# Kernel tuning notes

Hardware: AMD Instinct MI355X
Metric: run time of the kernel (lower is better)

The kernel has to match this reference:

```python
import jax, jax.numpy as jnp
import numpy as np

V, D, K = 400000, 300, 10

def setup_inputs() -> dict:
    key = jax.random.key(0)
    k1, k2 = jax.random.split(key)
    word2vec = jax.random.normal(k1, (V, D), dtype=jnp.float32)  # embedding table
    w = jax.random.normal(k2, (D,), dtype=jnp.float32)           # query vector
    return {"word2vec": word2vec, "w": w, "k": K}

def reference(word2vec, w, k):
    # cosine similarity: (word2vec @ w) / (||rows|| * ||w||), matching torch eps placement
    dots = word2vec @ w                                          # [V]
    row_norms = jnp.sqrt(jnp.sum(word2vec * word2vec, axis=1) + 1e-9)  # [V]
    q_norm = jnp.sqrt(jnp.sum(w * w))
    cos = dots / (row_norms * q_norm)                            # [V]
    vals, topk = jax.lax.top_k(cos, k)                           # top-k neighbors
    return vals, topk
```

## Files before the change

kernel.cpp:

```cpp
#include <hip/hip_runtime.h>

#define D    300
#define NF4  75
#define K    10
#define WPB  4
#define GPB  16
#define NBLOCKS 2048
#define CPT  20

__device__ __forceinline__ float d4(float4 a, float4 b) {
    return a.x*b.x + a.y*b.y + a.z*b.z + a.w*b.w;
}

__global__ __launch_bounds__(256) void cos_topk_partial(
    const float* __restrict__ emb, const float* __restrict__ wvec,
    float* __restrict__ cand_v, int* __restrict__ cand_i,
    int V, int totalGroups)
{
    const int tid  = threadIdx.x;
    const int lane = tid & 63;
    const int wid  = tid >> 6;
    const int l16  = lane & 15;
    const int rg   = lane >> 4;

    const float4* w4p = (const float4*)wvec;
    float4 w0 = w4p[l16];
    float4 w1 = w4p[l16 + 16];
    float4 w2 = w4p[l16 + 32];
    float4 w3 = w4p[l16 + 48];
    float4 w4t = make_float4(0.f, 0.f, 0.f, 0.f);
    if (l16 < NF4 - 64) w4t = w4p[l16 + 64];

    float qsq = d4(w0,w0) + d4(w1,w1) + d4(w2,w2) + d4(w3,w3) + d4(w4t,w4t);
    #pragma unroll
    for (int m = 8; m >= 1; m >>= 1) qsq += __shfl_xor(qsq, m, 64);
    const float qn = sqrtf(qsq);

    float tv[K]; int ti[K];
    #pragma unroll
    for (int j = 0; j < K; ++j) { tv[j] = -1e30f; ti[j] = 0; }

    const int g0 = (blockIdx.x * WPB + wid) * 4 + rg;
    for (int r = g0; r < V; r += totalGroups) {
        const float4* rp = (const float4*)(emb + (size_t)r * D);
        float4 a0 = rp[l16];
        float4 a1 = rp[l16 + 16];
        float4 a2 = rp[l16 + 32];
        float4 a3 = rp[l16 + 48];
        float4 a4 = make_float4(0.f, 0.f, 0.f, 0.f);
        if (l16 < NF4 - 64) a4 = rp[l16 + 64];

        float da = d4(a0, w0) + d4(a1, w1);
        float db = d4(a2, w2) + d4(a3, w3) + d4(a4, w4t);
        float sa = d4(a0, a0) + d4(a1, a1);
        float sb = d4(a2, a2) + d4(a3, a3) + d4(a4, a4);
        float dot = da + db;
        float sq  = sa + sb;

        #pragma unroll
        for (int m = 8; m >= 1; m >>= 1) {
            dot += __shfl_xor(dot, m, 64);
            sq  += __shfl_xor(sq,  m, 64);
        }
        float c = dot / (sqrtf(sq + 1e-9f) * qn);

        if (c > tv[K-1]) {
            tv[K-1] = c; ti[K-1] = r;
            #pragma unroll
            for (int j = K-1; j > 0; --j) {
                if (tv[j] > tv[j-1]) {
                    float t = tv[j]; tv[j] = tv[j-1]; tv[j-1] = t;
                    int   u = ti[j]; ti[j] = ti[j-1]; ti[j-1] = u;
                }
            }
        }
    }

    __shared__ float sv[GPB * K];
    __shared__ int   si[GPB * K];
    if (l16 == 0) {
        const int gidx = wid * 4 + rg;
        #pragma unroll
        for (int j = 0; j < K; ++j) { sv[gidx*K + j] = tv[j]; si[gidx*K + j] = ti[j]; }
    }
    __syncthreads();
    if (tid == 0) {
        float bv[K]; int bi[K];
        #pragma unroll
        for (int j = 0; j < K; ++j) { bv[j] = -1e30f; bi[j] = 0; }
        for (int t = 0; t < GPB * K; ++t) {
            float c = sv[t]; int r = si[t];
            if (c > bv[K-1]) {
                bv[K-1] = c; bi[K-1] = r;
                #pragma unroll
                for (int j = K-1; j > 0; --j) {
                    if (bv[j] > bv[j-1]) {
                        float t2 = bv[j]; bv[j] = bv[j-1]; bv[j-1] = t2;
                        int   u2 = bi[j]; bi[j] = bi[j-1]; bi[j-1] = u2;
                    }
                }
            }
        }
        #pragma unroll
        for (int j = 0; j < K; ++j) {
            cand_v[blockIdx.x*K + j] = bv[j];
            cand_i[blockIdx.x*K + j] = bi[j];
        }
    }
}

__global__ __launch_bounds__(1024) void topk_final(
    const float* __restrict__ cand_v, const int* __restrict__ cand_i,
    int nc, float* __restrict__ out)
{
    __shared__ float rv[16];
    __shared__ int   rp[16];
    __shared__ float s_bv;
    __shared__ int   s_bp;

    const int tid  = threadIdx.x;
    const int lane = tid & 63;
    const int wid  = tid >> 6;

    float v[CPT];
    #pragma unroll
    for (int t = 0; t < CPT; ++t) {
        int idx = tid + t * 1024;
        v[t] = (idx < nc) ? cand_v[idx] : -3e38f;
    }

    for (int p = 0; p < K; ++p) {
        float bestv = -3e38f; int bestpos = 0x7fffffff;
        #pragma unroll
        for (int t = 0; t < CPT; ++t) {
            if (v[t] > bestv) { bestv = v[t]; bestpos = tid + t * 1024; }
        }
        #pragma unroll
        for (int m = 32; m >= 1; m >>= 1) {
            float ov = __shfl_xor(bestv, m, 64);
            int   op = __shfl_xor(bestpos, m, 64);
            if (ov > bestv || (ov == bestv && op < bestpos)) { bestv = ov; bestpos = op; }
        }
        if (lane == 0) { rv[wid] = bestv; rp[wid] = bestpos; }
        __syncthreads();
        if (tid == 0) {
            float bv = rv[0]; int bp = rp[0];
            for (int i = 1; i < 16; ++i)
                if (rv[i] > bv || (rv[i] == bv && rp[i] < bp)) { bv = rv[i]; bp = rp[i]; }
            s_bv = bv; s_bp = bp;
            out[p]     = bv;
            out[K + p] = (float)cand_i[bp];
        }
        __syncthreads();
        const int wbp = s_bp;
        #pragma unroll
        for (int t = 0; t < CPT; ++t) {
            if (tid + t * 1024 == wbp) v[t] = -3e38f;
        }
        __syncthreads();
    }
}

extern "C" void kernel_launch(void* const* d_in, const int* in_sizes, int n_in,
                              void* d_out, int out_size, void* d_ws, size_t ws_size,
                              hipStream_t stream) {
    const float* emb  = (const float*)d_in[0];
    const float* wvec = (const float*)d_in[1];
    const int V = in_sizes[0] / D;

    int nblocks = NBLOCKS;
    size_t need = (size_t)nblocks * K * 8;
    if (need > ws_size) {
        nblocks = (int)(ws_size / (K * 8));
        if (nblocks < 1) nblocks = 1;
    }

    float* cand_v = (float*)d_ws;
    int*   cand_i = (int*)((float*)d_ws + (size_t)nblocks * K);

    cos_topk_partial<<<nblocks, 256, 0, stream>>>(emb, wvec, cand_v, cand_i,
                                                  V, nblocks * GPB);
    topk_final<<<1, 1024, 0, stream>>>(cand_v, cand_i, nblocks * K, (float*)d_out);
}
```

Before: 133.3 us.

## Split cosine scoring from top-k into three kernels with double-buffered row loads

The fused score-plus-top-k kernel is replaced by three kernels. The first writes every cosine score to workspace, prefetching the next row into registers while the current one is reduced. The second runs a block-level top-k over contiguous slices in 64 blocks, and the third merges 640 candidates. The aim is to strip the per-row insertion-sort branch out of the bandwidth-bound streaming loop and to overlap loads with compute. In exchange it adds a 1.6 MB score write and read-back plus an extra launch, and it assumes the workspace is large and V/s is at least 2.

```diff
diff --git a/kernel.cpp b/kernel.cpp
--- a/kernel.cpp
+++ b/kernel.cpp
@@ -6,22 +6,29 @@
 #define WPB  4
 #define GPB  16
 #define NBLOCKS 2048
-#define CPT  20
+#define NGROUPS (NBLOCKS * GPB)
+
+#define P2_BLOCKS  64
+#define P2_THREADS 1024
+#define P2_CPT     7
 
 __device__ __forceinline__ float d4(float4 a, float4 b) {
     return a.x*b.x + a.y*b.y + a.z*b.z + a.w*b.w;
 }
 
-__global__ __launch_bounds__(256) void cos_topk_partial(
+#define RED16(x) { x += __shfl_xor(x, 8, 64); x += __shfl_xor(x, 4, 64); \
+                   x += __shfl_xor(x, 2, 64); x += __shfl_xor(x, 1, 64); }
+
+__global__ __launch_bounds__(256) void cos_all(
     const float* __restrict__ emb, const float* __restrict__ wvec,
-    float* __restrict__ cand_v, int* __restrict__ cand_i,
-    int V, int totalGroups)
+    float* __restrict__ score, int V, int s)
 {
     const int tid  = threadIdx.x;
     const int lane = tid & 63;
     const int wid  = tid >> 6;
     const int l16  = lane & 15;
     const int rg   = lane >> 4;
+    const bool tl  = (l16 < NF4 - 64);
 
     const float4* w4p = (const float4*)wvec;
     float4 w0 = w4p[l16];
@@ -29,112 +36,151 @@
     float4 w2 = w4p[l16 + 32];
     float4 w3 = w4p[l16 + 48];
     float4 w4t = make_float4(0.f, 0.f, 0.f, 0.f);
-    if (l16 < NF4 - 64) w4t = w4p[l16 + 64];
-
-    float qsq = d4(w0,w0) + d4(w1,w1) + d4(w2,w2) + d4(w3,w3) + d4(w4t,w4t);
+    if (tl) w4t = w4p[l16 + 64];
+
+    float qsq = d4(w0,w0)+d4(w1,w1)+d4(w2,w2)+d4(w3,w3)+d4(w4t,w4t);
+    RED16(qsq);
+    const float qn = sqrtf(qsq);
+
+    const int g0 = (blockIdx.x * WPB + wid) * 4 + rg;
+    const size_t stepF4 = (size_t)s * NF4;
+
+    const float4* pA = (const float4*)emb + (size_t)g0 * NF4;
+    const float4* pB = pA + stepF4;
+
+    float4 A0,A1,A2,A3,A4, B0,B1,B2,B3,B4;
+    A4 = make_float4(0.f,0.f,0.f,0.f);
+    B4 = make_float4(0.f,0.f,0.f,0.f);
+
+#define LOADROW(P, C0,C1,C2,C3,C4) \
+    { C0 = (P)[l16]; C1 = (P)[l16+16]; C2 = (P)[l16+32]; C3 = (P)[l16+48]; \
+      if (tl) C4 = (P)[l16+64]; }
+
+#define DOTSQ(C0,C1,C2,C3,C4, DOT, SQ)                       \
+    float DOT, SQ;                                           \
+    {   float _da = d4(C0,w0) + d4(C1,w1);                   \
+        float _db = d4(C2,w2) + d4(C3,w3) + d4(C4,w4t);      \
+        float _sa = d4(C0,C0) + d4(C1,C1);                   \
+        float _sb = d4(C2,C2) + d4(C3,C3) + d4(C4,C4);       \
+        DOT = _da + _db; SQ = _sa + _sb; }
+
+#define FINISH(DOT, SQ, ROW)                                 \
+    { RED16(DOT); RED16(SQ);                                 \
+      float _c = DOT / (sqrtf(SQ + 1e-9f) * qn);             \
+      if (l16 == 0) score[ROW] = _c; }
+
+    LOADROW(pA, A0,A1,A2,A3,A4);
+    LOADROW(pB, B0,B1,B2,B3,B4);
+
+    int rowA = g0;
+    int rowB = g0 + s;
+    const int nfull = V / s;
+
+    for (int it = 0; it < nfull/2 - 1; ++it) {
+        {
+            DOTSQ(A0,A1,A2,A3,A4, dA, sA);
+            pA += 2*stepF4;
+            LOADROW(pA, A0,A1,A2,A3,A4);
+            FINISH(dA, sA, rowA);
+            rowA += 2*s;
+        }
+        {
+            DOTSQ(B0,B1,B2,B3,B4, dB, sB);
+            pB += 2*stepF4;
+            LOADROW(pB, B0,B1,B2,B3,B4);
+            FINISH(dB, sB, rowB);
+            rowB += 2*s;
+        }
+    }
+
+    {
+        DOTSQ(A0,A1,A2,A3,A4, dA, sA);
+        const bool hasTail = (rowA + 2*s) < V;
+        if (hasTail) { pA += 2*stepF4; LOADROW(pA, A0,A1,A2,A3,A4); }
+        FINISH(dA, sA, rowA);
+        {
+            DOTSQ(B0,B1,B2,B3,B4, dB, sB);
+            FINISH(dB, sB, rowB);
+        }
+        if (hasTail) {
+            DOTSQ(A0,A1,A2,A3,A4, dT, sT);
+            FINISH(dT, sT, rowA + 2*s);
+        }
+    }
+#undef LOADROW
+#undef DOTSQ
+#undef FINISH
+}
+
+__global__ __launch_bounds__(P2_THREADS) void block_topk(
+    const float* __restrict__ score, int V,
+    float* __restrict__ cand_v, int* __restrict__ cand_i)
+{
+    __shared__ float rv[16];
+    __shared__ int   rp[16];
+    __shared__ int   s_bp;
+
+    const int tid  = threadIdx.x;
+    const int lane = tid & 63;
+    const int wid  = tid >> 6;
+    const int per  = (V + gridDim.x - 1) / gridDim.x;
+    const int base = blockIdx.x * per;
+
+    float v[P2_CPT];
     #pragma unroll
-    for (int m = 8; m >= 1; m >>= 1) qsq += __shfl_xor(qsq, m, 64);
-    const float qn = sqrtf(qsq);
-
-    float tv[K]; int ti[K];
-    #pragma unroll
-    for (int j = 0; j < K; ++j) { tv[j] = -1e30f; ti[j] = 0; }
-
-    const int g0 = (blockIdx.x * WPB + wid) * 4 + rg;
-    for (int r = g0; r < V; r += totalGroups) {
-        const float4* rp = (const float4*)(emb + (size_t)r * D);
-        float4 a0 = rp[l16];
-        float4 a1 = rp[l16 + 16];
-        float4 a2 = rp[l16 + 32];
-        float4 a3 = rp[l16 + 48];
-        float4 a4 = make_float4(0.f, 0.f, 0.f, 0.f);
-        if (l16 < NF4 - 64) a4 = rp[l16 + 64];
-
-        float da = d4(a0, w0) + d4(a1, w1);
-        float db = d4(a2, w2) + d4(a3, w3) + d4(a4, w4t);
-        float sa = d4(a0, a0) + d4(a1, a1);
-        float sb = d4(a2, a2) + d4(a3, a3) + d4(a4, a4);
-        float dot = da + db;
-        float sq  = sa + sb;
-
-        #pragma unroll
-        for (int m = 8; m >= 1; m >>= 1) {
-            dot += __shfl_xor(dot, m, 64);
-            sq  += __shfl_xor(sq,  m, 64);
-        }
-        float c = dot / (sqrtf(sq + 1e-9f) * qn);
-
-        if (c > tv[K-1]) {
-            tv[K-1] = c; ti[K-1] = r;
-            #pragma unroll
-            for (int j = K-1; j > 0; --j) {
-                if (tv[j] > tv[j-1]) {
-                    float t = tv[j]; tv[j] = tv[j-1]; tv[j-1] = t;
-                    int   u = ti[j]; ti[j] = ti[j-1]; ti[j-1] = u;
-                }
-            }
-        }
-    }
-
-    __shared__ float sv[GPB * K];
-    __shared__ int   si[GPB * K];
-    if (l16 == 0) {
-        const int gidx = wid * 4 + rg;
-        #pragma unroll
-        for (int j = 0; j < K; ++j) { sv[gidx*K + j] = tv[j]; si[gidx*K + j] = ti[j]; }
-    }
-    __syncthreads();
-    if (tid == 0) {
-        float bv[K]; int bi[K];
-        #pragma unroll
-        for (int j = 0; j < K; ++j) { bv[j] = -1e30f; bi[j] = 0; }
-        for (int t = 0; t < GPB * K; ++t) {
-            float c = sv[t]; int r = si[t];
-            if (c > bv[K-1]) {
-                bv[K-1] = c; bi[K-1] = r;
-                #pragma unroll
-                for (int j = K-1; j > 0; --j) {
-                    if (bv[j] > bv[j-1]) {
-                        float t2 = bv[j]; bv[j] = bv[j-1]; bv[j-1] = t2;
-                        int   u2 = bi[j]; bi[j] = bi[j-1]; bi[j-1] = u2;
-                    }
-                }
-            }
-        }
-        #pragma unroll
-        for (int j = 0; j < K; ++j) {
-            cand_v[blockIdx.x*K + j] = bv[j];
-            cand_i[blockIdx.x*K + j] = bi[j];
-        }
-    }
-}
-
-__global__ __launch_bounds__(1024) void topk_final(
+    for (int t = 0; t < P2_CPT; ++t) {
+        int i = tid + t * P2_THREADS;
+        v[t] = (i < per && base + i < V) ? score[base + i] : -3e38f;
+    }
+
+    for (int p = 0; p < K; ++p) {
+        float bestv = -3e38f; int bestpos = 0x7fffffff;
+        #pragma unroll
+        for (int t = 0; t < P2_CPT; ++t) {
+            if (v[t] > bestv) { bestv = v[t]; bestpos = tid + t * P2_THREADS; }
+        }
+        #pragma unroll
+        for (int m = 32; m >= 1; m >>= 1) {
+            float ov = __shfl_xor(bestv, m, 64);
+            int   op = __shfl_xor(bestpos, m, 64);
+            if (ov > bestv || (ov == bestv && op < bestpos)) { bestv = ov; bestpos = op; }
+        }
+        if (lane == 0) { rv[wid] = bestv; rp[wid] = bestpos; }
+        __syncthreads();
+        if (tid == 0) {
+            float bv = rv[0]; int bp = rp[0];
+            for (int i = 1; i < 16; ++i)
+                if (rv[i] > bv || (rv[i] == bv && rp[i] < bp)) { bv = rv[i]; bp = rp[i]; }
+            cand_v[blockIdx.x*K + p] = bv;
+            cand_i[blockIdx.x*K + p] = base + bp;
+            s_bp = bp;
+        }
+        __syncthreads();
+        const int wbp = s_bp;
+        #pragma unroll
+        for (int t = 0; t < P2_CPT; ++t) {
+            if (tid + t * P2_THREADS == wbp) v[t] = -3e38f;
+        }
+        __syncthreads();
+    }
+}
+
+__global__ __launch_bounds__(P2_THREADS) void final_topk(
     const float* __restrict__ cand_v, const int* __restrict__ cand_i,
     int nc, float* __restrict__ out)
 {
     __shared__ float rv[16];
     __shared__ int   rp[16];
-    __shared__ float s_bv;
     __shared__ int   s_bp;
 
     const int tid  = threadIdx.x;
     const int lane = tid & 63;
     const int wid  = tid >> 6;
 
-    float v[CPT];
-    #pragma unroll
-    for (int t = 0; t < CPT; ++t) {
-        int idx = tid + t * 1024;
-        v[t] = (idx < nc) ? cand_v[idx] : -3e38f;
-    }
+    float v0 = (tid < nc) ? cand_v[tid] : -3e38f;
 
     for (int p = 0; p < K; ++p) {
-        float bestv = -3e38f; int bestpos = 0x7fffffff;
-        #pragma unroll
-        for (int t = 0; t < CPT; ++t) {
-            if (v[t] > bestv) { bestv = v[t]; bestpos = tid + t * 1024; }
-        }
+        float bestv = v0; int bestpos = tid;
         #pragma unroll
         for (int m = 32; m >= 1; m >>= 1) {
             float ov = __shfl_xor(bestv, m, 64);
@@ -147,16 +193,12 @@
             float bv = rv[0]; int bp = rp[0];
             for (int i = 1; i < 16; ++i)
                 if (rv[i] > bv || (rv[i] == bv && rp[i] < bp)) { bv = rv[i]; bp = rp[i]; }
-            s_bv = bv; s_bp = bp;
             out[p]     = bv;
             out[K + p] = (float)cand_i[bp];
-        }
-        __syncthreads();
-        const int wbp = s_bp;
-        #pragma unroll
-        for (int t = 0; t < CPT; ++t) {
-            if (tid + t * 1024 == wbp) v[t] = -3e38f;
-        }
+            s_bp = bp;
+        }
+        __syncthreads();
+        if (tid == s_bp) v0 = -3e38f;
         __syncthreads();
     }
 }
@@ -168,17 +210,11 @@
     const float* wvec = (const float*)d_in[1];
     const int V = in_sizes[0] / D;
 
-    int nblocks = NBLOCKS;
-    size_t need = (size_t)nblocks * K * 8;
-    if (need > ws_size) {
-        nblocks = (int)(ws_size / (K * 8));
-        if (nblocks < 1) nblocks = 1;
-    }
-
-    float* cand_v = (float*)d_ws;
-    int*   cand_i = (int*)((float*)d_ws + (size_t)nblocks * K);
-
-    cos_topk_partial<<<nblocks, 256, 0, stream>>>(emb, wvec, cand_v, cand_i,
-                                                  V, nblocks * GPB);
-    topk_final<<<1, 1024, 0, stream>>>(cand_v, cand_i, nblocks * K, (float*)d_out);
-}
+    float* score  = (float*)d_ws;
+    float* cand_v = score + V;
+    int*   cand_i = (int*)(cand_v + P2_BLOCKS * K);
+
+    cos_all<<<NBLOCKS, 256, 0, stream>>>(emb, wvec, score, V, NGROUPS);
+    block_topk<<<P2_BLOCKS, P2_THREADS, 0, stream>>>(score, V, cand_v, cand_i);
+    final_topk<<<1, P2_THREADS, 0, stream>>>(cand_v, cand_i, P2_BLOCKS * K, (float*)d_out);
+}
```

After: 133.4 us. Within noise of the previous version (+0.1%).
